# Kernel tuning notes

Hardware: AMD Instinct MI355X
Metric: run time of the kernel (lower is better)

The kernel has to match this reference:

```python
import jax, jax.numpy as jnp
import numpy as np

N = 100000
E = 1600000
D_IN = 128
D_OUT = 128
EPS = 1e-5


def setup_inputs() -> dict:
    key = jax.random.key(0)
    ks = jax.random.split(key, 8)
    x = jax.random.normal(ks[0], (N, D_IN), dtype=jnp.float32)
    edge_index = jax.random.randint(ks[1], (2, E), 0, N, dtype=jnp.int64)
    s1 = 1.0 / np.sqrt(D_IN)
    s2 = 1.0 / np.sqrt(D_OUT)
    W1 = jax.random.uniform(ks[2], (D_IN, D_OUT), jnp.float32, -s1, s1)
    b1 = jax.random.uniform(ks[3], (D_OUT,), jnp.float32, -s1, s1)
    W2 = jax.random.uniform(ks[4], (D_OUT, D_OUT), jnp.float32, -s2, s2)
    b2 = jax.random.uniform(ks[5], (D_OUT,), jnp.float32, -s2, s2)
    gamma = jnp.ones((D_OUT,), jnp.float32)
    beta = jnp.zeros((D_OUT,), jnp.float32)
    return {"x": x, "edge_index": edge_index, "W1": W1, "b1": b1,
            "W2": W2, "b2": b2, "gamma": gamma, "beta": beta}


def reference(x, edge_index, W1, b1, W2, b2, gamma, beta):
    row, col = edge_index[0], edge_index[1]
    # scatter-add neighbor aggregation: agg[row] += x[col]
    agg = jax.ops.segment_sum(x[col], row, num_segments=N)
    h = x + agg  # residual (self) + aggregated neighbors
    # MLP: Linear -> ReLU -> Linear -> BatchNorm1d (training-mode batch stats)
    h = jax.nn.relu(h @ W1 + b1)
    h = h @ W2 + b2
    mean = jnp.mean(h, axis=0)
    var = jnp.mean(jnp.square(h - mean), axis=0)  # biased var, as torch BN uses
    out = gamma * (h - mean) * jax.lax.rsqrt(var + EPS) + beta
    return out
```

## Files before the change

### kernel.cpp

```cpp
#include <hip/hip_runtime.h>

#define N_NODES 100000
#define N_EDGES 1600000
#define DIM     128
#define EPS_BN  1e-5f
#define NB      512
#define NPB     196
#define NBLK    256
#define EPB     6250
#define CAP     4096
#define M_TILE  64
#define M_PAD   100032
#define GBLK    1563
#define LPITCH  136

typedef __attribute__((ext_vector_type(8))) short short8;
typedef __attribute__((ext_vector_type(4))) float floatx4;

__device__ __forceinline__ unsigned short f2bf(float f) {
    unsigned u = __float_as_uint(f);
    return (unsigned short)((u + 0x7FFF + ((u >> 16) & 1)) >> 16);
}
__device__ __forceinline__ float bf2f(unsigned short b) {
    return __uint_as_float((unsigned)b << 16);
}

__device__ __forceinline__ int detect64(const void* eidx) {
    int v = ((const int*)eidx)[2 * (threadIdx.x & 63) + 1];
    unsigned long long b = __ballot(v != 0);
    return (b == 0ULL) ? 1 : 0;
}
__device__ __forceinline__ int load_row(const void* eidx, int is64, int e) {
    if (is64) return (int)((const long long*)eidx)[e];
    return ((const int*)eidx)[e];
}
__device__ __forceinline__ int load_col(const void* eidx, int is64, int e) {
    if (is64) return (int)((const long long*)eidx)[N_EDGES + e];
    return ((const int*)eidx)[N_EDGES + e];
}

__global__ void convert_w(const float* __restrict__ W1,
                          const float* __restrict__ W2,
                          unsigned short* __restrict__ W1t,
                          unsigned short* __restrict__ W2t,
                          int* __restrict__ bcur, float* __restrict__ gstats) {
    if (blockIdx.x == 2) {
        int t = threadIdx.x;
        if (t < NB) bcur[t] = 0;
        if (t < 256) { if (t < NB - 256) bcur[256 + t] = 0; }
        bcur[256 + threadIdx.x] = 0;
        if (t < 2 * DIM) gstats[t] = 0.f;
        return;
    }
    const float* W = blockIdx.x ? W2 : W1;
    unsigned short* Wt = blockIdx.x ? W2t : W1t;
    for (int i = threadIdx.x; i < DIM * DIM; i += 256) {
        int k = i >> 7, n = i & 127;
        Wt[n * DIM + k] = f2bf(W[i]);
    }
}

__global__ __launch_bounds__(256) void bin_scatter(const void* eidx, int* bcur,
                                                   unsigned* __restrict__ slots) {
    __shared__ int lh[NB];
    __shared__ int lbase[NB];
    __shared__ int loff[NB];
    __shared__ unsigned stage[EPB];
    __shared__ int gaddr[EPB];
    int t = threadIdx.x;
    int is64 = detect64(eidx);
    lh[t] = 0; lh[t + 256] = 0;
    __syncthreads();
    int base = blockIdx.x * EPB;
    for (int i = t; i < EPB; i += 256) {
        int r = load_row(eidx, is64, base + i);
        atomicAdd(&lh[r / NPB], 1);
    }
    __syncthreads();
    loff[t] = lh[t]; loff[t + 256] = lh[t + 256];
    __syncthreads();
    for (int off = 1; off < NB; off <<= 1) {
        int a0 = (t >= off) ? loff[t - off] : 0;
        int a1 = (t + 256 >= off) ? loff[t + 256 - off] : 0;
        __syncthreads();
        loff[t] += a0; loff[t + 256] += a1;
        __syncthreads();
    }
#pragma unroll
    for (int q = 0; q < 2; ++q) {
        int i = t + 256 * q;
        int c = lh[i];
        lbase[i] = c ? atomicAdd(&bcur[i], c) : 0;
        loff[i] -= c;
        lh[i] = 0;
    }
    __syncthreads();
    for (int i = t; i < EPB; i += 256) {
        int r = load_row(eidx, is64, base + i);
        int c = load_col(eidx, is64, base + i);
        int b = r / NPB;
        int pos = atomicAdd(&lh[b], 1);
        int idx = loff[b] + pos;
        stage[idx] = ((unsigned)(r - b * NPB) << 24) | (unsigned)c;
        gaddr[idx] = b * CAP + lbase[b] + pos;
    }
    __syncthreads();
    for (int i = t; i < EPB; i += 256)
        slots[gaddr[i]] = stage[i];
}

__global__ __launch_bounds__(256) void build_csr(const unsigned* __restrict__ slots,
                                                 const int* __restrict__ bcnt,
                                                 int* __restrict__ rowst,
                                                 int* __restrict__ cols) {
    __shared__ int tmp[NB];
    __shared__ int hist[256];
    __shared__ int excl[256];
    __shared__ int cur[256];
    __shared__ int colbuf[CAP];
    int t = threadIdx.x;
    int b = blockIdx.x;
    tmp[t] = bcnt[t]; tmp[t + 256] = bcnt[t + 256];
    __syncthreads();
    for (int off = 1; off < NB; off <<= 1) {
        int a0 = (t >= off) ? tmp[t - off] : 0;
        int a1 = (t + 256 >= off) ? tmp[t + 256 - off] : 0;
        __syncthreads();
        tmp[t] += a0; tmp[t + 256] += a1;
        __syncthreads();
    }
    int cnt = bcnt[b];
    int s = tmp[b] - cnt;
    int node0 = b * NPB;
    int nn = N_NODES - node0;
    if (nn > NPB) nn = NPB;
    const unsigned* pairs = slots + (size_t)b * CAP;
    hist[t] = 0;
    if (b == NB - 1 && t == 0) rowst[N_NODES] = N_EDGES;
    __syncthreads();
    for (int i = t; i < cnt; i += 256)
        atomicAdd(&hist[(int)(pairs[i] >> 24)], 1);
    __syncthreads();
    int v = hist[t];
    excl[t] = v;
    __syncthreads();
    for (int off = 1; off < 256; off <<= 1) {
        int a = (t >= off) ? excl[t - off] : 0;
        __syncthreads();
        excl[t] += a;
        __syncthreads();
    }
    int ex = excl[t] - v;
    if (t < nn) rowst[node0 + t] = s + ex;
    cur[t] = ex;
    __syncthreads();
    for (int i = t; i < cnt; i += 256) {
        unsigned pr = pairs[i];
        int pos = atomicAdd(&cur[pr >> 24], 1);
        colbuf[pos] = (int)(pr & 0xFFFFFFu);
    }
    __syncthreads();
    for (int i = t; i < cnt; i += 256) cols[s + i] = colbuf[i];
}

__global__ void xconv(const float* __restrict__ x,
                      unsigned short* __restrict__ xb) {
    int i = blockIdx.x * 256 + threadIdx.x;
    float4 v = ((const float4*)x)[i];
    ushort4 o;
    o.x = f2bf(v.x); o.y = f2bf(v.y); o.z = f2bf(v.z); o.w = f2bf(v.w);
    ((ushort4*)xb)[i] = o;
}

__global__ __launch_bounds__(256) void agg_kernel(
    const unsigned short* __restrict__ xb,
    const int* __restrict__ row_start, const int* __restrict__ cols,
    unsigned short* __restrict__ Hbf) {
    int wave = threadIdx.x >> 6;
    int lane = threadIdx.x & 63;
    int node = blockIdx.x * 4 + wave;
    const unsigned* xbw = (const unsigned*)xb;
    unsigned selfw = xbw[(size_t)node * 64 + lane];
    float2 acc;
    acc.x = __uint_as_float(selfw << 16);
    acc.y = __uint_as_float(selfw & 0xffff0000u);
    int s = row_start[node], e = row_start[node + 1];
    s = __builtin_amdgcn_readfirstlane(s);
    e = __builtin_amdgcn_readfirstlane(e);
    int d = e - s;
    if (d <= 16) {
        unsigned pw[16];
#pragma unroll
        for (int u = 0; u < 16; ++u) {
            int idx = s + u;
            int ci = (idx < e) ? idx : s;
            pw[u] = xbw[(size_t)cols[ci] * 64 + lane];
        }
#pragma unroll
        for (int u = 0; u < 16; ++u) {
            unsigned w = (u < d) ? pw[u] : 0u;
            acc.x += __uint_as_float(w << 16);
            acc.y += __uint_as_float(w & 0xffff0000u);
        }
    } else if (d <= 32) {
        unsigned pw[32];
#pragma unroll
        for (int u = 0; u < 32; ++u) {
            int idx = s + u;
            int ci = (idx < e) ? idx : s;
            pw[u] = xbw[(size_t)cols[ci] * 64 + lane];
        }
#pragma unroll
        for (int u = 0; u < 32; ++u) {
            unsigned w = (u < d) ? pw[u] : 0u;
            acc.x += __uint_as_float(w << 16);
            acc.y += __uint_as_float(w & 0xffff0000u);
        }
    } else {
        int j = s;
        for (; j + 16 <= e; j += 16) {
            unsigned pw[16];
#pragma unroll
            for (int u = 0; u < 16; ++u)
                pw[u] = xbw[(size_t)cols[j + u] * 64 + lane];
#pragma unroll
            for (int u = 0; u < 16; ++u) {
                acc.x += __uint_as_float(pw[u] << 16);
                acc.y += __uint_as_float(pw[u] & 0xffff0000u);
            }
        }
        for (; j < e; ++j) {
            unsigned pv = xbw[(size_t)cols[j] * 64 + lane];
            acc.x += __uint_as_float(pv << 16);
            acc.y += __uint_as_float(pv & 0xffff0000u);
        }
    }
    unsigned pack = (unsigned)f2bf(acc.x) | ((unsigned)f2bf(acc.y) << 16);
    ((unsigned*)Hbf)[(size_t)node * 64 + lane] = pack;
}

__global__ __launch_bounds__(256) void mlp_fused(
    const unsigned short* __restrict__ A,
    const unsigned short* __restrict__ B1t,
    const unsigned short* __restrict__ B2t,
    const float* __restrict__ bias1, const float* __restrict__ bias2,
    unsigned short* __restrict__ outb,
    float* __restrict__ gpart) {
    __shared__ unsigned short As[M_TILE * LPITCH];
    __shared__ unsigned short Bs[DIM * LPITCH];
    int t = threadIdx.x;
    int row0 = blockIdx.x * M_TILE;
    int lane = t & 63, wv = t >> 6;
    int m = lane & 15, g = lane >> 4;

#pragma unroll
    for (int i = 0; i < 4; ++i) {
        int ch = t + 256 * i;
        int r = ch >> 4, cc = ch & 15;
        *(uint4*)(&As[r * LPITCH + cc * 8]) =
            *(const uint4*)(&A[(size_t)(row0 + r) * DIM + cc * 8]);
    }
#pragma unroll
    for (int i = 0; i < 8; ++i) {
        int ch = t + 256 * i;
        int n = ch >> 4, cc = ch & 15;
        *(uint4*)(&Bs[n * LPITCH + cc * 8]) =
            *(const uint4*)(&B1t[n * DIM + cc * 8]);
    }
    __syncthreads();

    floatx4 acc1[8] = {};
#pragma unroll
    for (int kc = 0; kc < 4; ++kc) {
        short8 a = *(const short8*)(&As[(wv * 16 + m) * LPITCH + kc * 32 + g * 8]);
#pragma unroll
        for (int tt = 0; tt < 8; ++tt) {
            short8 b = *(const short8*)(&Bs[(tt * 16 + m) * LPITCH + kc * 32 + g * 8]);
            acc1[tt] = __builtin_amdgcn_mfma_f32_16x16x32_bf16(a, b, acc1[tt], 0, 0, 0);
        }
    }
    __syncthreads();

    uint4 wbuf[8];
#pragma unroll
    for (int i = 0; i < 8; ++i) {
        int ch = t + 256 * i;
        int n = ch >> 4, cc = ch & 15;
        wbuf[i] = *(const uint4*)(&B2t[n * DIM + cc * 8]);
    }
#pragma unroll
    for (int tt = 0; tt < 8; ++tt) {
        int col = tt * 16 + m;
        float bv = bias1[col];
#pragma unroll
        for (int j = 0; j < 4; ++j) {
            int rl = wv * 16 + g * 4 + j;
            As[rl * LPITCH + col] = f2bf(fmaxf(acc1[tt][j] + bv, 0.f));
        }
    }
#pragma unroll
    for (int i = 0; i < 8; ++i) {
        int ch = t + 256 * i;
        int n = ch >> 4, cc = ch & 15;
        *(uint4*)(&Bs[n * LPITCH + cc * 8]) = wbuf[i];
    }
    __syncthreads();

    floatx4 acc2[8] = {};
#pragma unroll
    for (int kc = 0; kc < 4; ++kc) {
        short8 a = *(const short8*)(&As[(wv * 16 + m) * LPITCH + kc * 32 + g * 8]);
#pragma unroll
        for (int tt = 0; tt < 8; ++tt) {
            short8 b = *(const short8*)(&Bs[(tt * 16 + m) * LPITCH + kc * 32 + g * 8]);
            acc2[tt] = __builtin_amdgcn_mfma_f32_16x16x32_bf16(a, b, acc2[tt], 0, 0, 0);
        }
    }

    float* csum = (float*)As;
    float* csq = csum + DIM;
    __syncthreads();
    if (t < DIM) { csum[t] = 0.f; csq[t] = 0.f; }
    __syncthreads();
#pragma unroll
    for (int tt = 0; tt < 8; ++tt) {
        int col = tt * 16 + m;
        float bv = bias2[col];
        float s = 0.f, q = 0.f;
#pragma unroll
        for (int j = 0; j < 4; ++j) {
            int row = row0 + wv * 16 + g * 4 + j;
            float v = acc2[tt][j] + bv;
            outb[(size_t)row * DIM + col] = f2bf(v);
            if (row < N_NODES) { s += v; q += v * v; }
        }
        atomicAdd(&csum[col], s);
        atomicAdd(&csq[col], q);
    }
    __syncthreads();
    gpart[(size_t)blockIdx.x * 256 + t] = (t < DIM) ? csum[t] : csq[t - DIM];
}

__global__ __launch_bounds__(256) void reduce_stats(
    const float* __restrict__ gpart, float* __restrict__ gstats) {
    int t = threadIdx.x;
    int chunk = (GBLK + 31) / 32;
    int r0 = blockIdx.x * chunk;
    int r1 = r0 + chunk < GBLK ? r0 + chunk : GBLK;
    float s = 0.f;
    for (int r = r0; r < r1; ++r) s += gpart[(size_t)r * 256 + t];
    atomicAdd(&gstats[t], s);
}

__global__ __launch_bounds__(256) void bn_apply(
    const unsigned short* __restrict__ H2, const float* __restrict__ gstats,
    const float* __restrict__ gamma, const float* __restrict__ beta,
    float* __restrict__ out) {
    __shared__ float sc_s[DIM], sh_s[DIM];
    int t = threadIdx.x;
    if (t < DIM) {
        float mean = gstats[t] * (1.0f / N_NODES);
        float m2 = gstats[DIM + t] * (1.0f / N_NODES);
        float var = m2 - mean * mean;
        float inv = rsqrtf(var + EPS_BN);
        float sc = gamma[t] * inv;
        sc_s[t] = sc;
        sh_s[t] = beta[t] - mean * sc;
    }
    __syncthreads();
    int i = blockIdx.x * 256 + t;
    int j4 = (i & 31) * 4;
    ushort4 hv = ((const ushort4*)H2)[i];
    float4 o;
    o.x = bf2f(hv.x) * sc_s[j4 + 0] + sh_s[j4 + 0];
    o.y = bf2f(hv.y) * sc_s[j4 + 1] + sh_s[j4 + 1];
    o.z = bf2f(hv.z) * sc_s[j4 + 2] + sh_s[j4 + 2];
    o.w = bf2f(hv.w) * sc_s[j4 + 3] + sh_s[j4 + 3];
    ((float4*)out)[i] = o;
}

extern "C" void kernel_launch(void* const* d_in, const int* in_sizes, int n_in,
                              void* d_out, int out_size, void* d_ws,
                              size_t ws_size, hipStream_t stream) {
    (void)in_sizes; (void)n_in; (void)out_size; (void)ws_size;
    const float* x     = (const float*)d_in[0];
    const void*  eidx  = d_in[1];
    const float* W1    = (const float*)d_in[2];
    const float* b1    = (const float*)d_in[3];
    const float* W2    = (const float*)d_in[4];
    const float* b2    = (const float*)d_in[5];
    const float* gamma = (const float*)d_in[6];
    const float* beta  = (const float*)d_in[7];
    float* out = (float*)d_out;

    char* p = (char*)d_ws;
    auto alloc = [&](size_t bytes) {
        char* r = p;
        p += (bytes + 255) & ~(size_t)255;
        return r;
    };
    unsigned short* Hbf  = (unsigned short*)alloc((size_t)M_PAD * DIM * 2);
    unsigned short* h2bf = (unsigned short*)alloc((size_t)M_PAD * DIM * 2);
    unsigned* slots = (unsigned*)h2bf;
    unsigned short* xb = (unsigned short*)alloc((size_t)N_NODES * DIM * 2);
    int*   cols   = (int*)alloc((size_t)(N_EDGES + 64) * 4);
    float* gpart  = (float*)alloc((size_t)GBLK * 256 * 4);
    int*   rowst  = (int*)alloc((size_t)(N_NODES + 1) * 4);
    int*   bcur   = (int*)alloc(NB * 4);
    unsigned short* W1t = (unsigned short*)alloc(DIM * DIM * 2);
    unsigned short* W2t = (unsigned short*)alloc(DIM * DIM * 2);
    float* gstats = (float*)alloc(2 * DIM * 4);

    convert_w<<<3, 256, 0, stream>>>(W1, W2, W1t, W2t, bcur, gstats);
    bin_scatter<<<NBLK, 256, 0, stream>>>(eidx, bcur, slots);
    build_csr<<<NB, 256, 0, stream>>>(slots, bcur, rowst, cols);

    xconv<<<N_NODES * DIM / 4 / 256, 256, 0, stream>>>(x, xb);
    agg_kernel<<<N_NODES / 4, 256, 0, stream>>>(xb, rowst, cols, Hbf);

    mlp_fused<<<GBLK, 256, 0, stream>>>(Hbf, W1t, W2t, b1, b2, h2bf, gpart);
    reduce_stats<<<32, 256, 0, stream>>>(gpart, gstats);
    bn_apply<<<(N_NODES * DIM / 4) / 256, 256, 0, stream>>>(h2bf, gstats,
                                                            gamma, beta, out);
}
```

Before: 312.0 us.

## Fuse x bf16 conversion into edge binning kernel and use finer bins

Doubles the number of destination bins to 1024, with half the nodes per bin and smaller capacity, and launches 1024 scatter blocks of about 1563 edges each for more parallelism. The standalone xconv kernel is removed and its fp32-to-bf16 conversion of x is done by a grid-stride loop at the end of the binning kernel, saving one launch. The prefix scans in binning and CSR build now cover 1024 entries, which adds scan work and more bin blocks per kernel. The per-bin capacity of 2048 is about 1.3x the expected edges per bin for random indices.

```diff
diff --git a/kernel.cpp b/kernel.cpp
--- a/kernel.cpp
+++ b/kernel.cpp
@@ -4,11 +4,11 @@
 #define N_EDGES 1600000
 #define DIM     128
 #define EPS_BN  1e-5f
-#define NB      512
-#define NPB     196
-#define NBLK    256
-#define EPB     6250
-#define CAP     4096
+#define NB      1024
+#define NPB     98
+#define NBLK    1024
+#define EPB     1563
+#define CAP     2048
 #define M_TILE  64
 #define M_PAD   100032
 #define GBLK    1563
@@ -46,9 +46,7 @@
                           int* __restrict__ bcur, float* __restrict__ gstats) {
     if (blockIdx.x == 2) {
         int t = threadIdx.x;
-        if (t < NB) bcur[t] = 0;
-        if (t < 256) { if (t < NB - 256) bcur[256 + t] = 0; }
-        bcur[256 + threadIdx.x] = 0;
+        bcur[t] = 0; bcur[t + 256] = 0; bcur[t + 512] = 0; bcur[t + 768] = 0;
         if (t < 2 * DIM) gstats[t] = 0.f;
         return;
     }
@@ -60,8 +58,9 @@
     }
 }
 
-__global__ __launch_bounds__(256) void bin_scatter(const void* eidx, int* bcur,
-                                                   unsigned* __restrict__ slots) {
+__global__ __launch_bounds__(256) void bin_scatter_x(
+    const void* eidx, int* bcur, unsigned* __restrict__ slots,
+    const float* __restrict__ x, unsigned short* __restrict__ xb) {
     __shared__ int lh[NB];
     __shared__ int lbase[NB];
     __shared__ int loff[NB];
@@ -69,25 +68,32 @@
     __shared__ int gaddr[EPB];
     int t = threadIdx.x;
     int is64 = detect64(eidx);
-    lh[t] = 0; lh[t + 256] = 0;
+    lh[t] = 0; lh[t + 256] = 0; lh[t + 512] = 0; lh[t + 768] = 0;
     __syncthreads();
     int base = blockIdx.x * EPB;
-    for (int i = t; i < EPB; i += 256) {
+    int cnt = N_EDGES - base;
+    if (cnt > EPB) cnt = EPB;
+    if (cnt < 0) cnt = 0;
+    for (int i = t; i < cnt; i += 256) {
         int r = load_row(eidx, is64, base + i);
         atomicAdd(&lh[r / NPB], 1);
     }
     __syncthreads();
     loff[t] = lh[t]; loff[t + 256] = lh[t + 256];
+    loff[t + 512] = lh[t + 512]; loff[t + 768] = lh[t + 768];
     __syncthreads();
     for (int off = 1; off < NB; off <<= 1) {
         int a0 = (t >= off) ? loff[t - off] : 0;
         int a1 = (t + 256 >= off) ? loff[t + 256 - off] : 0;
+        int a2 = (t + 512 >= off) ? loff[t + 512 - off] : 0;
+        int a3 = (t + 768 >= off) ? loff[t + 768 - off] : 0;
         __syncthreads();
         loff[t] += a0; loff[t + 256] += a1;
-        __syncthreads();
-    }
-#pragma unroll
-    for (int q = 0; q < 2; ++q) {
+        loff[t + 512] += a2; loff[t + 768] += a3;
+        __syncthreads();
+    }
+#pragma unroll
+    for (int q = 0; q < 4; ++q) {
         int i = t + 256 * q;
         int c = lh[i];
         lbase[i] = c ? atomicAdd(&bcur[i], c) : 0;
@@ -95,7 +101,7 @@
         lh[i] = 0;
     }
     __syncthreads();
-    for (int i = t; i < EPB; i += 256) {
+    for (int i = t; i < cnt; i += 256) {
         int r = load_row(eidx, is64, base + i);
         int c = load_col(eidx, is64, base + i);
         int b = r / NPB;
@@ -105,8 +111,14 @@
         gaddr[idx] = b * CAP + lbase[b] + pos;
     }
     __syncthreads();
-    for (int i = t; i < EPB; i += 256)
+    for (int i = t; i < cnt; i += 256)
         slots[gaddr[i]] = stage[i];
+    for (int i = blockIdx.x * 256 + t; i < N_NODES * DIM / 4; i += NBLK * 256) {
+        float4 v = ((const float4*)x)[i];
+        ushort4 o;
+        o.x = f2bf(v.x); o.y = f2bf(v.y); o.z = f2bf(v.z); o.w = f2bf(v.w);
+        ((ushort4*)xb)[i] = o;
+    }
 }
 
 __global__ __launch_bounds__(256) void build_csr(const unsigned* __restrict__ slots,
@@ -121,12 +133,16 @@
     int t = threadIdx.x;
     int b = blockIdx.x;
     tmp[t] = bcnt[t]; tmp[t + 256] = bcnt[t + 256];
+    tmp[t + 512] = bcnt[t + 512]; tmp[t + 768] = bcnt[t + 768];
     __syncthreads();
     for (int off = 1; off < NB; off <<= 1) {
         int a0 = (t >= off) ? tmp[t - off] : 0;
         int a1 = (t + 256 >= off) ? tmp[t + 256 - off] : 0;
+        int a2 = (t + 512 >= off) ? tmp[t + 512 - off] : 0;
+        int a3 = (t + 768 >= off) ? tmp[t + 768 - off] : 0;
         __syncthreads();
         tmp[t] += a0; tmp[t + 256] += a1;
+        tmp[t + 512] += a2; tmp[t + 768] += a3;
         __syncthreads();
     }
     int cnt = bcnt[b];
@@ -134,6 +150,7 @@
     int node0 = b * NPB;
     int nn = N_NODES - node0;
     if (nn > NPB) nn = NPB;
+    if (nn < 0) nn = 0;
     const unsigned* pairs = slots + (size_t)b * CAP;
     hist[t] = 0;
     if (b == NB - 1 && t == 0) rowst[N_NODES] = N_EDGES;
@@ -161,15 +178,6 @@
     }
     __syncthreads();
     for (int i = t; i < cnt; i += 256) cols[s + i] = colbuf[i];
-}
-
-__global__ void xconv(const float* __restrict__ x,
-                      unsigned short* __restrict__ xb) {
-    int i = blockIdx.x * 256 + threadIdx.x;
-    float4 v = ((const float4*)x)[i];
-    ushort4 o;
-    o.x = f2bf(v.x); o.y = f2bf(v.y); o.z = f2bf(v.z); o.w = f2bf(v.w);
-    ((ushort4*)xb)[i] = o;
 }
 
 __global__ __launch_bounds__(256) void agg_kernel(
@@ -412,10 +420,9 @@
     float* gstats = (float*)alloc(2 * DIM * 4);
 
     convert_w<<<3, 256, 0, stream>>>(W1, W2, W1t, W2t, bcur, gstats);
-    bin_scatter<<<NBLK, 256, 0, stream>>>(eidx, bcur, slots);
+    bin_scatter_x<<<NBLK, 256, 0, stream>>>(eidx, bcur, slots, x, xb);
     build_csr<<<NB, 256, 0, stream>>>(slots, bcur, rowst, cols);
 
-    xconv<<<N_NODES * DIM / 4 / 256, 256, 0, stream>>>(x, xb);
     agg_kernel<<<N_NODES / 4, 256, 0, stream>>>(xb, rowst, cols, Hbf);
 
     mlp_fused<<<GBLK, 256, 0, stream>>>(Hbf, W1t, W2t, b1, b2, h2bf, gpart);
```

New measurement: 326.8 us. 1.05x slower.
